# Optimization experiments

Hardware: AMD Instinct MI355X
Metric: run time of the kernel (lower is better)

Reference implementation:

```python
import jax, jax.numpy as jnp
import numpy as np

EMB_DIM = 1024
N_HEAD = 16
HEAD_SIZE = 64
B = 2
T = 2048


def setup_inputs() -> dict:
    key = jax.random.key(0)
    k_x, k_qkv, k_pw, k_pb = jax.random.split(key, 4)
    x = jax.random.normal(k_x, (B, T, EMB_DIM), dtype=jnp.float32)
    # nn.Linear(emb_dim, 3*emb_dim, bias=False): y = x @ W_qkv, W_qkv: [C, 3C]
    W_qkv = jax.random.normal(k_qkv, (EMB_DIM, 3 * EMB_DIM), dtype=jnp.float32) * (EMB_DIM ** -0.5)
    # nn.Linear(emb_dim, emb_dim) with bias
    W_proj = jax.random.normal(k_pw, (EMB_DIM, EMB_DIM), dtype=jnp.float32) * (EMB_DIM ** -0.5)
    b_proj = jax.random.normal(k_pb, (EMB_DIM,), dtype=jnp.float32) * 0.01
    return {"x": x, "W_qkv": W_qkv, "W_proj": W_proj, "b_proj": b_proj}


def reference(x, W_qkv, W_proj, b_proj):
    Bn, Tn, C = x.shape
    qkv = x @ W_qkv                          # [B, T, 3C]
    q, k, v = jnp.split(qkv, 3, axis=-1)
    # [B, T, H, D] -> attention over heads via einsum (no explicit transpose)
    q = q.reshape(Bn, Tn, N_HEAD, HEAD_SIZE)
    k = k.reshape(Bn, Tn, N_HEAD, HEAD_SIZE)
    v = v.reshape(Bn, Tn, N_HEAD, HEAD_SIZE)
    att = jnp.einsum("bthd,bshd->bhts", q, k) * (HEAD_SIZE ** -0.5)  # [B, H, T, T]
    causal = jnp.tril(jnp.ones((Tn, Tn), dtype=bool))
    att = jnp.where(causal, att, -jnp.inf)
    att = jax.nn.softmax(att, axis=-1)
    y = jnp.einsum("bhts,bshd->bthd", att, v).reshape(Bn, Tn, C)
    return y @ W_proj + b_proj
```

## Files before the change

### kernel.cpp

```cpp
#include <hip/hip_runtime.h>
#include <hip/hip_bf16.h>

typedef unsigned short u16;
typedef unsigned int u32;
typedef u16 u16x4 __attribute__((ext_vector_type(4)));
typedef u16 u16x8 __attribute__((ext_vector_type(8)));
typedef u32 u32x4 __attribute__((ext_vector_type(4)));
typedef __bf16 bf16x8 __attribute__((ext_vector_type(8)));
typedef float f32x4 __attribute__((ext_vector_type(4)));

__device__ __forceinline__ u16 f2bf(float f) {
  union { float f; unsigned u; } v; v.f = f;
  unsigned r = v.u + 0x7fffu + ((v.u >> 16) & 1u);
  return (u16)(r >> 16);
}

__device__ __forceinline__ u16 bf(float f) {
  __bf16 h = (__bf16)f;
  union { __bf16 h; u16 u; } c; c.h = h;
  return c.u;
}

__device__ __forceinline__ u32 pack2(float lo, float hi) {
  return (u32)bf(lo) | ((u32)bf(hi) << 16);
}

__device__ __forceinline__ float fexp2(float x) {
#if __has_builtin(__builtin_amdgcn_exp2f)
  return __builtin_amdgcn_exp2f(x);
#else
  return exp2f(x);
#endif
}

__device__ __forceinline__ float frcp(float x) {
#if __has_builtin(__builtin_amdgcn_rcpf)
  return __builtin_amdgcn_rcpf(x);
#else
  return 1.0f / x;
#endif
}

__device__ __forceinline__ void gload16(const void* g, void* l) {
  __builtin_amdgcn_global_load_lds((const __attribute__((address_space(1))) void*)g,
                                   (__attribute__((address_space(3))) void*)l, 16, 0, 0);
}

__global__ __launch_bounds__(256) void prep(
    const float* __restrict__ x, const float* __restrict__ Wqkv,
    const float* __restrict__ Wproj, u16* __restrict__ xb,
    u16* __restrict__ wqT, u16* __restrict__ wpT)
{
  __shared__ float tile[32][33];
  const int bid = blockIdx.x;
  if (bid < 2048) {
    int i = (bid * 256 + threadIdx.x) * 8;
    f32x4 a = *(const f32x4*)(x + i);
    f32x4 b = *(const f32x4*)(x + i + 4);
    u16x8 r;
    r[0] = f2bf(a[0]); r[1] = f2bf(a[1]); r[2] = f2bf(a[2]); r[3] = f2bf(a[3]);
    r[4] = f2bf(b[0]); r[5] = f2bf(b[1]); r[6] = f2bf(b[2]); r[7] = f2bf(b[3]);
    *(u16x8*)(xb + i) = r;
    return;
  }
  int flat = bid - 2048;
  int bx = flat & 127, by = flat >> 7;
  const float* in;
  u16* out;
  int N;
  if (bx < 96) { in = Wqkv; out = wqT; N = 3072; }
  else         { in = Wproj; out = wpT; N = 1024; bx -= 96; }
  const int K = 1024;
  int n0 = bx * 32, k0 = by * 32;
  int tx = threadIdx.x & 31, ty = threadIdx.x >> 5;
  for (int i = 0; i < 32; i += 8)
    tile[ty + i][tx] = in[(long)(k0 + ty + i) * N + n0 + tx];
  __syncthreads();
  for (int i = 0; i < 32; i += 8)
    out[(long)(n0 + ty + i) * K + k0 + tx] = f2bf(tile[tx][ty + i]);
}

template<int BM, int BN, bool F32OUT>
__global__ __launch_bounds__(256) void gemm_bt(
    const u16* __restrict__ A, const u16* __restrict__ Bt,
    void* __restrict__ Cp, const float* __restrict__ bias,
    int M, int N, int K)
{
  constexpr int MR = BM / 32, NR = BN / 32;
  constexpr int RA = BM / 32, RB = BN / 32;
  __shared__ char lds[(BM + BN) * 128];
  char* As = lds;
  char* Bs = lds + BM * 128;
  const int tid = threadIdx.x;
  const int l = tid & 63, w = tid >> 6;
  const int wr = w >> 1, wc = w & 1;
  const int lr = l & 15, q4 = l >> 4;
  const long row0 = (long)blockIdx.x * BM;
  const long col0 = (long)blockIdx.y * BN;

  f32x4 acc[MR][NR] = {};

  const u16* gA[RA];
  int oA[RA];
  for (int i = 0; i < RA; ++i) {
    int cc = i * 256 + tid;
    int r = cc >> 3, c = (cc & 7) ^ (r & 7);
    oA[i] = cc * 16;
    gA[i] = A + (row0 + r) * K + c * 8;
  }
  const u16* gB[RB];
  int oB[RB];
  for (int i = 0; i < RB; ++i) {
    int cc = i * 256 + tid;
    int r = cc >> 3, c = (cc & 7) ^ (r & 7);
    oB[i] = cc * 16;
    gB[i] = Bt + (col0 + r) * K + c * 8;
  }

  for (int k0 = 0; k0 < K; k0 += 64) {
    __syncthreads();
    for (int i = 0; i < RA; ++i) gload16(gA[i] + k0, As + oA[i]);
    for (int i = 0; i < RB; ++i) gload16(gB[i] + k0, Bs + oB[i]);
    __syncthreads();
    for (int kk = 0; kk < 2; ++kk) {
      bf16x8 a[MR], b[NR];
      for (int m = 0; m < MR; ++m) {
        int r = wr * (BM / 2) + m * 16 + lr;
        a[m] = *(const bf16x8*)(As + r * 128 + (((kk * 4 + q4) ^ (r & 7)) << 4));
      }
      for (int n = 0; n < NR; ++n) {
        int r = wc * (BN / 2) + n * 16 + lr;
        b[n] = *(const bf16x8*)(Bs + r * 128 + (((kk * 4 + q4) ^ (r & 7)) << 4));
      }
      for (int m = 0; m < MR; ++m)
        for (int n = 0; n < NR; ++n)
          acc[m][n] = __builtin_amdgcn_mfma_f32_16x16x32_bf16(a[m], b[n], acc[m][n], 0, 0, 0);
    }
  }

  for (int n = 0; n < NR; ++n) {
    int col = (int)col0 + wc * (BN / 2) + n * 16 + lr;
    float bv = 0.f;
    if (F32OUT) bv = bias[col];
    for (int m = 0; m < MR; ++m) {
      for (int reg = 0; reg < 4; ++reg) {
        long row = row0 + wr * (BM / 2) + m * 16 + q4 * 4 + reg;
        float vv = acc[m][n][reg] + bv;
        if (F32OUT) ((float*)Cp)[row * N + col] = vv;
        else        ((u16*)Cp)[row * N + col] = f2bf(vv);
      }
    }
  }
}

#define FXOR(d) (((((d) & 7) ^ (((d) >> 3) & 7))) << 4)

#define VSCAT(vtb, ra, rb)                                                     \
  for (int j = 0; j < 4; ++j) {                                                \
    int d = vd0 + j;                                                           \
    *(u32*)((vtb) + d * 128 + (vcol2 ^ FXOR(d))) = (u32)(ra)[j] | ((u32)(rb)[j] << 16); \
  }

#define COMPUTE_TILE(T)                                                        \
  if (64 * (T) <= wrow + 15) {                                                 \
    char* ks_ = ksmem + ((T) & 3) * 8192;                                      \
    char* vt_ = vtmem + ((T) & 3) * 8192;                                      \
    const int k0_ = 64 * (T);                                                  \
    f32x4 st[4] = {};                                                          \
    __builtin_amdgcn_s_setprio(1);                                             \
    for (int kk = 0; kk < 2; ++kk)                                             \
      for (int n = 0; n < 4; ++n) {                                            \
        int r = n * 16 + lr;                                                   \
        int c = (kk * 4 + g) ^ (r & 7);                                        \
        bf16x8 kf = *(const bf16x8*)(ks_ + r * 128 + (c << 4));                \
        st[n] = __builtin_amdgcn_mfma_f32_16x16x32_bf16(kf, qf[kk], st[n], 0, 0, 0); \
      }                                                                        \
    __builtin_amdgcn_s_setprio(0);                                             \
    if (k0_ + 63 > wrow) {                                                     \
      for (int n = 0; n < 4; ++n)                                              \
        for (int reg = 0; reg < 4; ++reg)                                      \
          if (k0_ + n * 16 + g * 4 + reg > wrow + lr)                          \
            st[n][reg] = -__builtin_inff();                                    \
    }                                                                          \
    u32 pk[4][2];                                                              \
    for (int n = 0; n < 4; ++n) {                                              \
      float p0 = fexp2(st[n][0]), p1 = fexp2(st[n][1]);                        \
      float p2 = fexp2(st[n][2]), p3 = fexp2(st[n][3]);                        \
      pk[n][0] = pack2(p0, p1);                                                \
      pk[n][1] = pack2(p2, p3);                                                \
    }                                                                          \
    __builtin_amdgcn_s_setprio(1);                                             \
    for (int kt = 0; kt < 2; ++kt) {                                           \
      u32x4 pb;                                                                \
      pb[0] = pk[2 * kt][0]; pb[1] = pk[2 * kt][1];                            \
      pb[2] = pk[2 * kt + 1][0]; pb[3] = pk[2 * kt + 1][1];                    \
      bf16x8 pf = *(bf16x8*)&pb;                                               \
      for (int n = 0; n < 4; ++n) {                                            \
        int dd = n * 16 + lr;                                                  \
        bf16x8 vf = *(const bf16x8*)(vt_ + dd * 128 + ((kt * 64 + g * 16) ^ FXOR(dd))); \
        o[n] = __builtin_amdgcn_mfma_f32_16x16x32_bf16(vf, pf, o[n], 0, 0, 0); \
      }                                                                        \
      ls = __builtin_amdgcn_mfma_f32_16x16x32_bf16(ones, pf, ls, 0, 0, 0);     \
    }                                                                          \
    __builtin_amdgcn_s_setprio(0);                                             \
  }

__global__ __launch_bounds__(512) void attn_fwd(
    const u16* __restrict__ qkv, u16* __restrict__ atty)
{
  __shared__ char ksmem[4 * 8192];
  __shared__ char vtmem[4 * 8192];
  const int tid = threadIdx.x;
  const int l = tid & 63, w = tid >> 6;
  const int lr = l & 15, g = l >> 4;
  const int xh = blockIdx.x;
  const int h = xh & 15;
  const long base = (long)(xh >> 4) * 2048;
  const int y = blockIdx.y;
  const int ti = (y < 8) ? y : (23 - y);
  const int wrow = (w < 4) ? (ti * 64 + w * 16) : ((31 - ti) * 64 + (w - 4) * 16);

  bf16x8 qf[2];
  for (int kk = 0; kk < 2; ++kk) {
    u16x8 raw = *(const u16x8*)(qkv + (base + wrow + lr) * 3072 + h * 64 + kk * 32 + g * 8);
    u16x8 sc;
    for (int j = 0; j < 8; ++j) {
      union { unsigned u; float f; } c; c.u = ((unsigned)raw[j]) << 16;
      sc[j] = bf(c.f * 0.18033688f);
    }
    qf[kk] = *(bf16x8*)&sc;
  }

  f32x4 ls = {};
  f32x4 o[4] = {};
  u32x4 onesu = {0x3F803F80u, 0x3F803F80u, 0x3F803F80u, 0x3F803F80u};
  bf16x8 ones = *(bf16x8*)&onesu;

  const int kr = tid >> 3, kc = (tid & 7) ^ (kr & 7);
  const u16* kg = qkv + (base + kr) * 3072 + 1024 + h * 64 + kc * 8;
  const int va = tid >> 4;
  const int vd0 = (tid & 15) * 4;
  const int vk0 = va * 2;
  const int vn = vk0 >> 4, vgp2 = (vk0 >> 2) & 3, vr = vk0 & 3;
  const int vcol2 = ((vn >> 1) * 32 + vgp2 * 8 + (vn & 1) * 4 + vr) * 2;
  const u16* vgp = qkv + (base + vk0) * 3072 + 2048 + h * 64 + vd0;

  const int nkv = 32 - ti;

  {
    u16x4 a0 = *(const u16x4*)(vgp);
    u16x4 b0 = *(const u16x4*)(vgp + 3072);
    u16x4 a1 = *(const u16x4*)(vgp + 196608);
    u16x4 b1 = *(const u16x4*)(vgp + 196608 + 3072);
    gload16(kg, ksmem + tid * 16);
    gload16(kg + 196608, ksmem + 8192 + tid * 16);
    VSCAT(vtmem, a0, b0);
    VSCAT(vtmem + 8192, a1, b1);
  }
  __syncthreads();

  for (int tb = 0; tb < nkv; tb += 2) {
    u16x4 p2a, p2b, p3a, p3b;
    const bool pf2 = (tb + 2) < nkv, pf3 = (tb + 3) < nkv;
    if (pf2) {
      long off = (long)(tb + 2) * 196608;
      p2a = *(const u16x4*)(vgp + off);
      p2b = *(const u16x4*)(vgp + off + 3072);
      gload16(kg + off, ksmem + ((tb + 2) & 3) * 8192 + tid * 16);
    }
    if (pf3) {
      long off = (long)(tb + 3) * 196608;
      p3a = *(const u16x4*)(vgp + off);
      p3b = *(const u16x4*)(vgp + off + 3072);
      gload16(kg + off, ksmem + ((tb + 3) & 3) * 8192 + tid * 16);
    }

    COMPUTE_TILE(tb);
    if (tb + 1 < nkv) COMPUTE_TILE(tb + 1);

    if (pf2) VSCAT(vtmem + ((tb + 2) & 3) * 8192, p2a, p2b);
    if (pf3) VSCAT(vtmem + ((tb + 3) & 3) * 8192, p3a, p3b);
    __syncthreads();
  }

  float inv = frcp(ls[0]);
  long row = base + wrow + lr;
  for (int n = 0; n < 4; ++n) {
    u16x4 ov;
    for (int reg = 0; reg < 4; ++reg) ov[reg] = bf(o[n][reg] * inv);
    *(u16x4*)(atty + row * 1024 + h * 64 + n * 16 + g * 4) = ov;
  }
}

extern "C" void kernel_launch(void* const* d_in, const int* in_sizes, int n_in,
                              void* d_out, int out_size, void* d_ws, size_t ws_size,
                              hipStream_t stream) {
  const float* x     = (const float*)d_in[0];
  const float* Wqkv  = (const float*)d_in[1];
  const float* Wproj = (const float*)d_in[2];
  const float* bproj = (const float*)d_in[3];
  char* ws = (char*)d_ws;
  u16* xb   = (u16*)(ws);
  u16* wqT  = (u16*)(ws + 8388608);
  u16* wpT  = (u16*)(ws + 14680064);
  u16* qkv  = (u16*)(ws + 16777216);
  u16* atty = (u16*)(ws + 41943040);

  prep<<<6144, 256, 0, stream>>>(x, Wqkv, Wproj, xb, wqT, wpT);
  gemm_bt<128, 192, false><<<dim3(32, 16), 256, 0, stream>>>(xb, wqT, (void*)qkv, nullptr, 4096, 3072, 1024);
  attn_fwd<<<dim3(32, 16), 512, 0, stream>>>(qkv, atty);
  gemm_bt<128, 64, true><<<dim3(32, 16), 256, 0, stream>>>(atty, wpT, d_out, bproj, 4096, 1024, 1024);
}
```

Before: 97.42 us.

## Switch attention KV pipeline to triple-buffered one-tile-per-iteration rotation

Replaces the 4-slot LDS ring that processed two KV tiles per barrier with a 3-slot rotating buffer that processes one tile per iteration while prefetching the tile two ahead. This cuts LDS usage from 64KB to 48KB and lowers register pressure, since only one tile's V values are held in flight. The trade-off is twice as many __syncthreads barriers per KV sweep and less compute between barriers to hide load latency.

Result: faster. 95.30 us, median of 2 (-2.2%).

```diff
diff --git a/kernel.cpp b/kernel.cpp
--- a/kernel.cpp
+++ b/kernel.cpp
@@ -161,10 +161,8 @@
     *(u32*)((vtb) + d * 128 + (vcol2 ^ FXOR(d))) = (u32)(ra)[j] | ((u32)(rb)[j] << 16); \
   }
 
-#define COMPUTE_TILE(T)                                                        \
+#define COMPUTE_TILE(T, KS, VT)                                                \
   if (64 * (T) <= wrow + 15) {                                                 \
-    char* ks_ = ksmem + ((T) & 3) * 8192;                                      \
-    char* vt_ = vtmem + ((T) & 3) * 8192;                                      \
     const int k0_ = 64 * (T);                                                  \
     f32x4 st[4] = {};                                                          \
     __builtin_amdgcn_s_setprio(1);                                             \
@@ -172,7 +170,7 @@
       for (int n = 0; n < 4; ++n) {                                            \
         int r = n * 16 + lr;                                                   \
         int c = (kk * 4 + g) ^ (r & 7);                                        \
-        bf16x8 kf = *(const bf16x8*)(ks_ + r * 128 + (c << 4));                \
+        bf16x8 kf = *(const bf16x8*)((KS) + r * 128 + (c << 4));               \
         st[n] = __builtin_amdgcn_mfma_f32_16x16x32_bf16(kf, qf[kk], st[n], 0, 0, 0); \
       }                                                                        \
     __builtin_amdgcn_s_setprio(0);                                             \
@@ -197,7 +195,7 @@
       bf16x8 pf = *(bf16x8*)&pb;                                               \
       for (int n = 0; n < 4; ++n) {                                            \
         int dd = n * 16 + lr;                                                  \
-        bf16x8 vf = *(const bf16x8*)(vt_ + dd * 128 + ((kt * 64 + g * 16) ^ FXOR(dd))); \
+        bf16x8 vf = *(const bf16x8*)((VT) + dd * 128 + ((kt * 64 + g * 16) ^ FXOR(dd))); \
         o[n] = __builtin_amdgcn_mfma_f32_16x16x32_bf16(vf, pf, o[n], 0, 0, 0); \
       }                                                                        \
       ls = __builtin_amdgcn_mfma_f32_16x16x32_bf16(ones, pf, ls, 0, 0, 0);     \
@@ -208,8 +206,8 @@
 __global__ __launch_bounds__(512) void attn_fwd(
     const u16* __restrict__ qkv, u16* __restrict__ atty)
 {
-  __shared__ char ksmem[4 * 8192];
-  __shared__ char vtmem[4 * 8192];
+  __shared__ char ksmem[3 * 8192];
+  __shared__ char vtmem[3 * 8192];
   const int tid = threadIdx.x;
   const int l = tid & 63, w = tid >> 6;
   const int lr = l & 15, g = l >> 4;
@@ -259,28 +257,26 @@
   }
   __syncthreads();
 
-  for (int tb = 0; tb < nkv; tb += 2) {
-    u16x4 p2a, p2b, p3a, p3b;
-    const bool pf2 = (tb + 2) < nkv, pf3 = (tb + 3) < nkv;
-    if (pf2) {
-      long off = (long)(tb + 2) * 196608;
-      p2a = *(const u16x4*)(vgp + off);
-      p2b = *(const u16x4*)(vgp + off + 3072);
-      gload16(kg + off, ksmem + ((tb + 2) & 3) * 8192 + tid * 16);
+  char* kA = ksmem;         char* vA = vtmem;
+  char* kB = ksmem + 8192;  char* vB = vtmem + 8192;
+  char* kC = ksmem + 16384; char* vC = vtmem + 16384;
+
+  for (int t = 0; t < nkv; ++t) {
+    u16x4 pva, pvb;
+    const bool pf = (t + 2) < nkv;
+    if (pf) {
+      long off = (long)(t + 2) * 196608;
+      pva = *(const u16x4*)(vgp + off);
+      pvb = *(const u16x4*)(vgp + off + 3072);
+      gload16(kg + off, kC + tid * 16);
     }
-    if (pf3) {
-      long off = (long)(tb + 3) * 196608;
-      p3a = *(const u16x4*)(vgp + off);
-      p3b = *(const u16x4*)(vgp + off + 3072);
-      gload16(kg + off, ksmem + ((tb + 3) & 3) * 8192 + tid * 16);
-    }
-
-    COMPUTE_TILE(tb);
-    if (tb + 1 < nkv) COMPUTE_TILE(tb + 1);
-
-    if (pf2) VSCAT(vtmem + ((tb + 2) & 3) * 8192, p2a, p2b);
-    if (pf3) VSCAT(vtmem + ((tb + 3) & 3) * 8192, p3a, p3b);
+
+    COMPUTE_TILE(t, kA, vA);
+
+    if (pf) VSCAT(vC, pva, pvb);
     __syncthreads();
+    char* tk = kA; kA = kB; kB = kC; kC = tk;
+    char* tv = vA; vA = vB; vB = vC; vC = tv;
   }
 
   float inv = frcp(ls[0]);
```
